# Performance work log

Measured on AMD Instinct MI355X. Metric: run time of the kernel, lower is better.

The kernel has to match this reference:

```python
import jax, jax.numpy as jnp
import numpy as np

B, L, C, H, W = 2, 3, 64, 32, 32
DI, N, DT_RANK, K = 128, 16, 4, 4  # d_inner=2*C, d_state, dt_rank=ceil(C/16), 4 scan dirs


def setup_inputs() -> dict:
    key = jax.random.key(0)
    ks = iter(jax.random.split(key, 48))
    nrm = lambda shape, s=0.02: jax.random.normal(next(ks), shape, jnp.float32) * s
    return {
        "image_sequence": jax.random.normal(next(ks), (B, L, C, H, W), jnp.float32),
        "difficult_zone": jax.random.normal(next(ks), (B, C, H, W), jnp.float32),
        "sigma": jax.random.uniform(next(ks), (B, C, H, W), jnp.float32),
        # LayerNorm2d applied to each frame
        "norm_g": jnp.ones((C,)), "norm_b": jnp.zeros((C,)),
        # ConvolutionalResBlock (in=3C -> out=C), GroupNorm(num_groups=1)
        "gn1_g": jnp.ones((3 * C,)), "gn1_b": jnp.zeros((3 * C,)),
        "conv1_w": nrm((C, 3 * C, 3, 3)), "conv1_b": jnp.zeros((C,)),
        "gn2_g": jnp.ones((C,)), "gn2_b": jnp.zeros((C,)),
        "conv2_w": nrm((C, C, 3, 3)), "conv2_b": jnp.zeros((C,)),
        "skip_w": nrm((C, 3 * C, 1, 1)), "skip_b": jnp.zeros((C,)),
        # VSSBlock pre-norms
        "ln1_g": jnp.ones((C,)), "ln1_b": jnp.zeros((C,)),
        "ln2_g": jnp.ones((C,)), "ln2_b": jnp.zeros((C,)),
        # SS2D
        "in_proj_w": nrm((2 * DI, C)),
        "dwconv_w": nrm((DI, 1, 3, 3)), "dwconv_b": jnp.zeros((DI,)),
        "x_proj_w": nrm((K, DT_RANK + 2 * N, DI)),
        "dt_proj_w": nrm((K, DI, DT_RANK), 0.1),
        "dt_proj_b": jnp.log(jnp.expm1(jnp.full((K, DI), 0.01, jnp.float32))),
        "A_logs": jnp.log(jnp.tile(jnp.arange(1, N + 1, dtype=jnp.float32), (K * DI, 1))),
        "Ds": jnp.ones((K * DI,)),
        "out_norm_g": jnp.ones((DI,)), "out_norm_b": jnp.zeros((DI,)),
        "out_proj_w": nrm((C, DI)),
        # Mlp (hidden = C)
        "fc1_w": nrm((C, C)), "fc1_b": jnp.zeros((C,)),
        "fc2_w": nrm((C, C)), "fc2_b": jnp.zeros((C,)),
    }


def _ln(x, g, b, eps=1e-5):  # layernorm over last axis
    m = x.mean(-1, keepdims=True)
    v = x.var(-1, keepdims=True)
    return (x - m) * jax.lax.rsqrt(v + eps) * g + b


def _ln2d(x, g, b, eps=1e-6):  # per-pixel channel layernorm, NCHW
    m = x.mean(1, keepdims=True)
    v = x.var(1, keepdims=True)
    return (x - m) * jax.lax.rsqrt(v + eps) * g[None, :, None, None] + b[None, :, None, None]


def _gn1(x, g, b, eps=1e-5):  # GroupNorm(num_groups=1), NCHW
    m = x.mean((1, 2, 3), keepdims=True)
    v = x.var((1, 2, 3), keepdims=True)
    return (x - m) * jax.lax.rsqrt(v + eps) * g[None, :, None, None] + b[None, :, None, None]


def _conv(x, w, b, pad):
    y = jax.lax.conv_general_dilated(x, w, (1, 1), [(pad, pad), (pad, pad)],
                                     dimension_numbers=("NCHW", "OIHW", "NCHW"))
    return y + b[None, :, None, None]


def _forward(image_sequence, difficult_zone, sigma, norm_g, norm_b, gn1_g, gn1_b,
             conv1_w, conv1_b, gn2_g, gn2_b, conv2_w, conv2_b, skip_w, skip_b,
             ln1_g, ln1_b, ln2_g, ln2_b, in_proj_w, dwconv_w, dwconv_b, x_proj_w,
             dt_proj_w, dt_proj_b, A_logs, Ds, out_norm_g, out_norm_b, out_proj_w,
             fc1_w, fc1_b, fc2_w, fc2_b):
    b, l, c, h, w = image_sequence.shape
    bl, L2 = b * l, h * w
    # fold frame loop into batch (identical math per frame in the torch loop)
    frames = _ln2d(image_sequence.reshape(bl, c, h, w), norm_g, norm_b)
    dz = jnp.broadcast_to(difficult_zone[:, None], (b, l, c, h, w)).reshape(bl, c, h, w)
    sg = jnp.broadcast_to(sigma[:, None], (b, l, c, h, w)).reshape(bl, c, h, w)
    x = jnp.concatenate([dz, frames, sg], axis=1)  # [bl, 3c, h, w]
    # channel compressor: pre-act conv res block
    hdn = _conv(jax.nn.silu(_gn1(x, gn1_g, gn1_b)), conv1_w, conv1_b, 1)
    hdn = _conv(jax.nn.silu(_gn1(hdn, gn2_g, gn2_b)), conv2_w, conv2_b, 1)
    x = hdn + _conv(x, skip_w, skip_b, 0)          # [bl, c, h, w]
    x = x.transpose(0, 2, 3, 1)                    # [bl, h, w, c]
    # --- VSSBlock (pre-norm): x = x + SS2D(LN(x)) ---
    xn = _ln(x, ln1_g, ln1_b)
    xz = xn @ in_proj_w.T                          # [bl,h,w,2*DI]
    xc, z = jnp.split(xz, 2, axis=-1)
    xc = xc.transpose(0, 3, 1, 2)                  # [bl, DI, h, w]
    xc = jax.lax.conv_general_dilated(xc, dwconv_w, (1, 1), [(1, 1), (1, 1)],
                                      dimension_numbers=("NCHW", "OIHW", "NCHW"),
                                      feature_group_count=DI) + dwconv_b[None, :, None, None]
    xc = jax.nn.silu(xc)
    # 4-direction scan inputs (HW, WH, and their reverses)
    xf = xc.reshape(bl, DI, L2)
    xt = xc.transpose(0, 1, 3, 2).reshape(bl, DI, L2)
    xs = jnp.stack([xf, xt], axis=1)
    xs = jnp.concatenate([xs, jnp.flip(xs, axis=-1)], axis=1)  # [bl, 4, DI, L2]
    x_dbl = jnp.einsum("bkdl,kcd->bkcl", xs, x_proj_w)
    dts, Bs, Cs = jnp.split(x_dbl, [DT_RANK, DT_RANK + N], axis=2)
    dts = jnp.einsum("bkrl,kdr->bkdl", dts, dt_proj_w) + dt_proj_b[None, :, :, None]
    dts = jax.nn.softplus(dts)                     # [bl, 4, DI, L2]
    A = -jnp.exp(A_logs).reshape(K, DI, N)
    dA = jnp.exp(dts[..., None] * A[None, :, :, None, :])            # [bl,4,DI,L2,N]
    dBu = dts[..., None] * Bs.transpose(0, 1, 3, 2)[:, :, None] * xs[..., None]
    a_t = dA.transpose(3, 0, 1, 2, 4)              # [L2, bl, 4, DI, N]
    bu_t = dBu.transpose(3, 0, 1, 2, 4)
    c_t = Cs.transpose(3, 0, 1, 2)                 # [L2, bl, 4, N]

    def step(hid, inp):
        a_i, bu_i, c_i = inp
        hid = a_i * hid + bu_i
        return hid, jnp.einsum("bkdn,bkn->bkd", hid, c_i)

    h0 = jnp.zeros((bl, K, DI, N), xs.dtype)
    _, ys = jax.lax.scan(step, h0, (a_t, bu_t, c_t))                 # [L2, bl, 4, DI]
    ys = ys.transpose(1, 2, 3, 0) + xs * Ds.reshape(K, DI)[None, :, :, None]
    inv = jnp.flip(ys[:, 2:4], axis=-1)
    y = (ys[:, 0] + inv[:, 0]
         + ys[:, 1].reshape(bl, DI, w, h).transpose(0, 1, 3, 2).reshape(bl, DI, L2)
         + inv[:, 1].reshape(bl, DI, w, h).transpose(0, 1, 3, 2).reshape(bl, DI, L2))
    y = _ln(y.transpose(0, 2, 1), out_norm_g, out_norm_b).reshape(bl, h, w, DI)
    y = y * jax.nn.silu(z)
    x = x + y @ out_proj_w.T
    # --- x = x + Mlp(LN(x)) ---
    xn = _ln(x, ln2_g, ln2_b)
    x = x + (jax.nn.gelu(xn @ fc1_w.T + fc1_b, approximate=False) @ fc2_w.T + fc2_b)
    return x.transpose(0, 3, 1, 2).reshape(b, l, c, h, w)


def reference(image_sequence, difficult_zone, sigma, norm_g, norm_b, gn1_g, gn1_b,
              conv1_w, conv1_b, gn2_g, gn2_b, conv2_w, conv2_b, skip_w, skip_b,
              ln1_g, ln1_b, ln2_g, ln2_b, in_proj_w, dwconv_w, dwconv_b, x_proj_w,
              dt_proj_w, dt_proj_b, A_logs, Ds, out_norm_g, out_norm_b, out_proj_w,
              fc1_w, fc1_b, fc2_w, fc2_b):
    return _forward(image_sequence, difficult_zone, sigma, norm_g, norm_b, gn1_g, gn1_b,
                    conv1_w, conv1_b, gn2_g, gn2_b, conv2_w, conv2_b, skip_w, skip_b,
                    ln1_g, ln1_b, ln2_g, ln2_b, in_proj_w, dwconv_w, dwconv_b, x_proj_w,
                    dt_proj_w, dt_proj_b, A_logs, Ds, out_norm_g, out_norm_b, out_proj_w,
                    fc1_w, fc1_b, fc2_w, fc2_b)
```

## Files before the change

kernel.cpp:

```cpp
#include <hip/hip_runtime.h>
#include <math.h>

#define BL    6
#define CCH   64
#define C3    192
#define L2    1024
#define DIC   128
#define NST   16
#define K4    4
#define PSTR  1088
#define NCH   32

#define LOG2E 1.44269504088896340736f
#define LN2C  0.69314718055994530942f

typedef float f2 __attribute__((ext_vector_type(2)));
__device__ __forceinline__ f2 mkf2(float a, float b){ f2 r; r.x=a; r.y=b; return r; }
__device__ __forceinline__ f2 fma2(f2 a, float b, f2 c){
  f2 bb; bb.x=b; bb.y=b;
  return __builtin_elementwise_fma(a, bb, c);
}

__device__ __forceinline__ float fexp(float x){ return __builtin_amdgcn_exp2f(x*LOG2E); }
__device__ __forceinline__ float fsilu(float x){ return x * __builtin_amdgcn_rcpf(1.f + fexp(-x)); }
__device__ __forceinline__ float fsoftplus(float x){
  if (x > 20.f) return x;
  return __builtin_amdgcn_logf(1.f + fexp(x)) * LN2C;
}
__device__ __forceinline__ float fgelu(float x){
  return 0.5f*x*(1.f + erff(x*0.70710678118654752440f));
}

__global__ __launch_bounds__(256) void k_ln2d(const float* __restrict__ img,
    const float* __restrict__ dz, const float* __restrict__ sg,
    const float* __restrict__ g, const float* __restrict__ b, float* __restrict__ x3c,
    float* __restrict__ psum1, float* __restrict__ psq1){
  __shared__ float ps[4][8], pq[4][8], gs[4], gq[4];
  int s = blockIdx.x >> 7;
  int pg = blockIdx.x & 127;
  int tid = threadIdx.x;
  int px = tid & 7; int cg = tid >> 3;
  int wv = tid >> 6; int lane = tid & 63;
  int p = pg*8 + px;
  int bsmp = s/3;
  const float* fr = img + (size_t)s*CCH*L2;
  float vals[2]; float sm=0.f, sq=0.f;
  #pragma unroll
  for (int j=0;j<2;++j){
    int c = cg*2 + j;
    float v = fr[c*L2 + p];
    vals[j]=v; sm+=v; sq+=v*v;
  }
  sm += __shfl_xor(sm,8,64);  sq += __shfl_xor(sq,8,64);
  sm += __shfl_xor(sm,16,64); sq += __shfl_xor(sq,16,64);
  sm += __shfl_xor(sm,32,64); sq += __shfl_xor(sq,32,64);
  if (lane < 8){ ps[wv][lane]=sm; pq[wv][lane]=sq; }
  __syncthreads();
  sm = ps[0][px]+ps[1][px]+ps[2][px]+ps[3][px];
  sq = pq[0][px]+pq[1][px]+pq[2][px]+pq[3][px];
  float mean = sm*(1.f/CCH); float var = sq*(1.f/CCH)-mean*mean;
  float rs = rsqrtf(var + 1e-6f);
  float* o = x3c + (size_t)s*C3*L2;
  const float* dzp = dz + (size_t)bsmp*CCH*L2;
  const float* sgp = sg + (size_t)bsmp*CCH*L2;
  float gsm=0.f, gsq=0.f;
  #pragma unroll
  for (int j=0;j<2;++j){
    int c = cg*2+j;
    float dzv = dzp[c*L2+p];
    float nv  = (vals[j]-mean)*rs*g[c] + b[c];
    float sgv = sgp[c*L2+p];
    o[c*L2+p] = dzv;
    o[(CCH+c)*L2+p] = nv;
    o[(2*CCH+c)*L2+p] = sgv;
    gsm += dzv+nv+sgv; gsq += dzv*dzv+nv*nv+sgv*sgv;
  }
  for (int m=1;m<64;m<<=1){ gsm+=__shfl_xor(gsm,m,64); gsq+=__shfl_xor(gsq,m,64); }
  if (lane==0){ gs[wv]=gsm; gq[wv]=gsq; }
  __syncthreads();
  if (tid==0){
    psum1[blockIdx.x] = gs[0]+gs[1]+gs[2]+gs[3];
    psq1 [blockIdx.x] = gq[0]+gq[1]+gq[2]+gq[3];
  }
}

__global__ __launch_bounds__(256) void k_gnact1_skip(const float* __restrict__ x3c,
    const float* __restrict__ psum, const float* __restrict__ psq,
    const float* __restrict__ g, const float* __restrict__ b,
    const float* __restrict__ wsk,
    float* __restrict__ xact1, float* __restrict__ part){
  int bx = blockIdx.x;
  int tid = threadIdx.x;
  if (bx < 1152){
    int s = bx / C3; int c = bx % C3;
    float sm=0.f, sq=0.f;
    for (int i=0;i<128;++i){ sm += psum[s*128+i]; sq += psq[s*128+i]; }
    float mean = sm*(1.f/(C3*L2));
    float var = sq*(1.f/(C3*L2)) - mean*mean;
    float rs = rsqrtf(var + 1e-5f);
    float gc = g[c]*rs; float bc = b[c] - mean*rs*g[c];
    float4 v = *(const float4*)(x3c + (size_t)bx*1024 + tid*4);
    float4 o; o.x = fsilu(v.x*gc+bc); o.y = fsilu(v.y*gc+bc);
    o.z = fsilu(v.z*gc+bc); o.w = fsilu(v.w*gc+bc);
    float* pl = xact1 + (size_t)bx*PSTR;
    *(float4*)(pl + 32 + tid*4) = o;
    float4 z4 = make_float4(0.f,0.f,0.f,0.f);
    if (tid < 8)  *(float4*)(pl + tid*4) = z4;
    else if (tid < 16) *(float4*)(pl + 1056 + (tid-8)*4) = z4;
  } else {
    int t = bx - 1152;
    int role = t & 1; int cop = (t>>1)&31; int s = t >> 6;
    int co0 = cop*2, co1 = co0+1;
    int row = tid>>3; int q = tid&7; int col0 = q*4;
    int p = row*32+col0;
    f2 a[4];
    #pragma unroll
    for (int i=0;i<4;++i){ a[i].x=0.f; a[i].y=0.f; }
    int ci0 = role*96;
    const float* x3 = x3c + ((size_t)s*C3 + ci0)*L2 + p;
    const float* w0p = wsk + co0*C3 + ci0;
    const float* w1p = wsk + co1*C3 + ci0;
    #pragma unroll 4
    for (int ci=0; ci<96; ++ci){
      float4 v = *(const float4*)(x3 + (size_t)ci*L2);
      f2 w = mkf2(w0p[ci], w1p[ci]);
      a[0] = fma2(w, v.x, a[0]);
      a[1] = fma2(w, v.y, a[1]);
      a[2] = fma2(w, v.z, a[2]);
      a[3] = fma2(w, v.w, a[3]);
    }
    float* pp = part + (size_t)(4+role)*(BL*CCH*L2) + ((size_t)s*CCH+co0)*L2 + p;
    *(float4*)pp = make_float4(a[0].x,a[1].x,a[2].x,a[3].x);
    *(float4*)(pp+L2) = make_float4(a[0].y,a[1].y,a[2].y,a[3].y);
  }
}

__global__ __launch_bounds__(256) void k_gnact_pad(const float* __restrict__ x,
    const float* __restrict__ psum, const float* __restrict__ psq,
    const float* __restrict__ g, const float* __restrict__ b,
    int ch, int parts, float inv_n, float eps, float* __restrict__ out){
  int bx = blockIdx.x;
  int s = bx / ch; int c = bx % ch;
  int tid = threadIdx.x;
  float sm=0.f, sq=0.f;
  for (int i=0;i<parts;++i){ sm += psum[s*parts+i]; sq += psq[s*parts+i]; }
  float mean = sm*inv_n;
  float var = sq*inv_n - mean*mean;
  float rs = rsqrtf(var + eps);
  float gc = g[c]*rs; float bc = b[c] - mean*rs*g[c];
  float4 v = *(const float4*)(x + (size_t)bx*1024 + tid*4);
  float4 o; o.x = fsilu(v.x*gc+bc); o.y = fsilu(v.y*gc+bc);
  o.z = fsilu(v.z*gc+bc); o.w = fsilu(v.w*gc+bc);
  float* pl = out + (size_t)bx*PSTR;
  *(float4*)(pl + 32 + tid*4) = o;
  float4 z4 = make_float4(0.f,0.f,0.f,0.f);
  if (tid < 8)  *(float4*)(pl + tid*4) = z4;
  else if (tid < 16) *(float4*)(pl + 1056 + (tid-8)*4) = z4;
}

__device__ __forceinline__ void conv_row_acc2(f2* a, float4 mid, float lf, float rt,
    const float* wp0, const float* wp1){
  f2 w0 = mkf2(wp0[0],wp1[0]);
  f2 w1 = mkf2(wp0[1],wp1[1]);
  f2 w2 = mkf2(wp0[2],wp1[2]);
  a[0] = fma2(w0,lf,   fma2(w1,mid.x, fma2(w2,mid.y, a[0])));
  a[1] = fma2(w0,mid.x,fma2(w1,mid.y, fma2(w2,mid.z, a[1])));
  a[2] = fma2(w0,mid.y,fma2(w1,mid.z, fma2(w2,mid.w, a[2])));
  a[3] = fma2(w0,mid.z,fma2(w1,mid.w, fma2(w2,rt,    a[3])));
}

__device__ __forceinline__ void conv_ci_body2(float4 m0, float4 m1, float4 m2, int q,
    const float* wp0, const float* wp1, f2* a){
  float lf0=__shfl_up(m0.w,1,64), rt0=__shfl_down(m0.x,1,64);
  float lf1=__shfl_up(m1.w,1,64), rt1=__shfl_down(m1.x,1,64);
  float lf2=__shfl_up(m2.w,1,64), rt2=__shfl_down(m2.x,1,64);
  if (q==0){ lf0=0.f; lf1=0.f; lf2=0.f; }
  if (q==7){ rt0=0.f; rt1=0.f; rt2=0.f; }
  conv_row_acc2(a,m0,lf0,rt0, wp0+0, wp1+0);
  conv_row_acc2(a,m1,lf1,rt1, wp0+3, wp1+3);
  conv_row_acc2(a,m2,lf2,rt2, wp0+6, wp1+6);
}

__global__ __launch_bounds__(256) void k_conv1_split(const float* __restrict__ xact,
    const float* __restrict__ w, float* __restrict__ part){
  int bx = blockIdx.x; int kk = bx % 12; int r = bx / 12;
  int cop = r & 31; int s = r >> 5;
  int co0 = cop*2, co1 = co0+1;
  int tid = threadIdx.x; int row = tid>>3; int q = tid&7; int col0 = q*4;
  f2 a[4];
  #pragma unroll
  for (int i=0;i<4;++i){ a[i].x=0.f; a[i].y=0.f; }
  int ci0 = kk*16;
  const float* pl = xact + ((size_t)s*C3 + ci0)*PSTR + row*32 + col0;
  const float* wp0 = w + (size_t)(co0*C3 + ci0)*9;
  const float* wp1 = w + (size_t)(co1*C3 + ci0)*9;
  float4 m0 = *(const float4*)(pl);
  float4 m1 = *(const float4*)(pl+32);
  float4 m2 = *(const float4*)(pl+64);
  #pragma unroll 2
  for (int i=0;i<16;++i){
    const float* pn = pl + (i<15 ? PSTR : 0);
    float4 n0 = *(const float4*)(pn);
    float4 n1 = *(const float4*)(pn+32);
    float4 n2 = *(const float4*)(pn+64);
    conv_ci_body2(m0,m1,m2,q, wp0, wp1, a);
    wp0 += 9; wp1 += 9; pl = pn; m0=n0; m1=n1; m2=n2;
  }
  float* pp = part + (size_t)kk*(BL*CCH*L2) + ((size_t)s*CCH+co0)*L2 + row*32+col0;
  *(float4*)pp = make_float4(a[0].x,a[1].x,a[2].x,a[3].x);
  *(float4*)(pp+L2) = make_float4(a[0].y,a[1].y,a[2].y,a[3].y);
}

__global__ __launch_bounds__(256) void k_reduce1(const float* __restrict__ part,
    const float* __restrict__ bias, float* __restrict__ h1,
    float* __restrict__ psum2, float* __restrict__ psq2){
  int co = blockIdx.x & 63; int s = blockIdx.x >> 6;
  size_t ofs = ((size_t)s*CCH+co)*L2 + threadIdx.x*4;
  const size_t stride = (size_t)BL*CCH*L2;
  float4 acc = *(const float4*)(part + ofs);
  #pragma unroll
  for (int kk=1;kk<12;++kk){
    float4 r = *(const float4*)(part + (size_t)kk*stride + ofs);
    acc.x += r.x; acc.y += r.y; acc.z += r.z; acc.w += r.w;
  }
  float bv = bias[co];
  acc.x += bv; acc.y += bv; acc.z += bv; acc.w += bv;
  *(float4*)(h1 + ofs) = acc;
  float sm = acc.x+acc.y+acc.z+acc.w;
  float sq = acc.x*acc.x+acc.y*acc.y+acc.z*acc.z+acc.w*acc.w;
  for (int m=1;m<64;m<<=1){ sm+=__shfl_xor(sm,m,64); sq+=__shfl_xor(sq,m,64); }
  __shared__ float s_sm[4], s_sq[4];
  int wv = threadIdx.x>>6;
  if ((threadIdx.x&63)==0){ s_sm[wv]=sm; s_sq[wv]=sq; }
  __syncthreads();
  if (threadIdx.x==0){
    psum2[blockIdx.x] = s_sm[0]+s_sm[1]+s_sm[2]+s_sm[3];
    psq2 [blockIdx.x] = s_sq[0]+s_sq[1]+s_sq[2]+s_sq[3];
  }
}

__global__ __launch_bounds__(256) void k_conv2_split(const float* __restrict__ xact2,
    const float* __restrict__ w2, float* __restrict__ part){
  int bx = blockIdx.x; int role = bx & 3; int t = bx >> 2;
  int cop = t & 31; int s = t >> 5;
  int co0 = cop*2, co1 = co0+1;
  int tid = threadIdx.x; int row = tid>>3; int q = tid&7; int col0 = q*4;
  int p = row*32+col0;
  f2 a[4];
  #pragma unroll
  for (int i=0;i<4;++i){ a[i].x=0.f; a[i].y=0.f; }
  int ci0 = role*16;
  const float* pl = xact2 + ((size_t)s*CCH + ci0)*PSTR + row*32 + col0;
  const float* wp0 = w2 + (size_t)(co0*CCH + ci0)*9;
  const float* wp1 = w2 + (size_t)(co1*CCH + ci0)*9;
  float4 m0 = *(const float4*)(pl);
  float4 m1 = *(const float4*)(pl+32);
  float4 m2 = *(const float4*)(pl+64);
  #pragma unroll 2
  for (int i=0;i<16;++i){
    const float* pn = pl + (i<15 ? PSTR : 0);
    float4 n0 = *(const float4*)(pn);
    float4 n1 = *(const float4*)(pn+32);
    float4 n2 = *(const float4*)(pn+64);
    conv_ci_body2(m0,m1,m2,q, wp0, wp1, a);
    wp0 += 9; wp1 += 9; pl = pn; m0=n0; m1=n1; m2=n2;
  }
  float* pp = part + (size_t)role*(BL*CCH*L2) + ((size_t)s*CCH+co0)*L2 + p;
  *(float4*)pp = make_float4(a[0].x,a[1].x,a[2].x,a[3].x);
  *(float4*)(pp+L2) = make_float4(a[0].y,a[1].y,a[2].y,a[3].y);
}

__global__ __launch_bounds__(256) void k_red2_ln1_inproj(const float* __restrict__ part,
    const float* __restrict__ b2, const float* __restrict__ bsk,
    const float* __restrict__ g, const float* __restrict__ b,
    const float* __restrict__ W,
    float* __restrict__ x_cmaj, float* __restrict__ xc, float* __restrict__ z_t){
  __shared__ float xn_s[64*65];
  int bx = blockIdx.x; int oq = bx & 7; int pg = (bx>>3)&15; int s = bx>>7;
  int p0 = pg*64;
  int tid = threadIdx.x;
  const size_t stride = (size_t)BL*CCH*L2;
  #pragma unroll
  for (int kq=0;kq<4;++kq){
    int f = kq*256 + tid;
    int co = f >> 4; int px4 = (f & 15)*4;
    size_t ofs = ((size_t)s*CCH+co)*L2 + p0 + px4;
    float4 r0 = *(const float4*)(part + ofs);
    float4 r1 = *(const float4*)(part + stride + ofs);
    float4 r2 = *(const float4*)(part + 2*stride + ofs);
    float4 r3 = *(const float4*)(part + 3*stride + ofs);
    float4 r4 = *(const float4*)(part + 4*stride + ofs);
    float4 r5 = *(const float4*)(part + 5*stride + ofs);
    float bv = b2[co]+bsk[co];
    float4 o;
    o.x = ((r0.x+r1.x)+(r2.x+r3.x))+(r4.x+r5.x)+bv;
    o.y = ((r0.y+r1.y)+(r2.y+r3.y))+(r4.y+r5.y)+bv;
    o.z = ((r0.z+r1.z)+(r2.z+r3.z))+(r4.z+r5.z)+bv;
    o.w = ((r0.w+r1.w)+(r2.w+r3.w))+(r4.w+r5.w)+bv;
    if (oq == 0) *(float4*)(x_cmaj + ofs) = o;
    xn_s[(px4+0)*65 + co] = o.x;
    xn_s[(px4+1)*65 + co] = o.y;
    xn_s[(px4+2)*65 + co] = o.z;
    xn_s[(px4+3)*65 + co] = o.w;
  }
  __syncthreads();
  {
    int wv = __builtin_amdgcn_readfirstlane(tid>>6); int lane = tid&63;
    for (int j=0;j<16;++j){
      int pl = wv*16 + j;
      float v = xn_s[pl*65 + lane];
      float sm = v, sq = v*v;
      for (int m=1;m<64;m<<=1){ sm += __shfl_xor(sm,m,64); sq += __shfl_xor(sq,m,64); }
      float mean = sm*(1.f/64.f); float var = sq*(1.f/64.f) - mean*mean;
      float rs = rsqrtf(var + 1e-5f);
      xn_s[pl*65 + lane] = (v-mean)*rs*g[lane] + b[lane];
    }
  }
  __syncthreads();
  int px_l = tid & 63;
  int og = __builtin_amdgcn_readfirstlane(tid >> 6);
  int o0 = oq*32 + og*8;
  f2 acc[4];
  #pragma unroll
  for (int oi=0;oi<4;++oi){ acc[oi].x=0.f; acc[oi].y=0.f; }
  for (int c=0;c<64;++c){
    float xv = xn_s[px_l*65 + c];
    #pragma unroll
    for (int oi=0;oi<4;++oi)
      acc[oi] = fma2(mkf2(W[(o0+2*oi)*64 + c], W[(o0+2*oi+1)*64 + c]), xv, acc[oi]);
  }
  int p = p0 + px_l;
  if (oq < 4){
    #pragma unroll
    for (int oi=0;oi<4;++oi){
      xc[((size_t)s*DIC + o0 + 2*oi)*L2 + p]   = acc[oi].x;
      xc[((size_t)s*DIC + o0 + 2*oi+1)*L2 + p] = acc[oi].y;
    }
  } else {
    #pragma unroll
    for (int oi=0;oi<4;++oi){
      z_t[((size_t)s*DIC + (o0-128) + 2*oi)*L2 + p]   = acc[oi].x;
      z_t[((size_t)s*DIC + (o0-128) + 2*oi+1)*L2 + p] = acc[oi].y;
    }
  }
}

__global__ __launch_bounds__(256) void k_xproj_dt(const float* __restrict__ xc,
    const float* __restrict__ dww, const float* __restrict__ dwb,
    const float* __restrict__ W,
    float* __restrict__ dtr, float* __restrict__ Bp, float* __restrict__ Cp,
    float* __restrict__ u_t){
  __shared__ float smem[128*68];
  int bx = blockIdx.x; int pg = bx & 15; int sk = bx >> 4;
  int k = sk & 3; int s = sk >> 2;
  int tid = threadIdx.x;
  for (int i = tid; i < 128*16; i += 256){
    int dr = i>>4; int j4 = (i&15)*4;
    int rw = j4>>5; int col0 = j4 & 31;
    int gr = pg*2 + rw;
    int q = i&7;
    const float* xr = xc + ((size_t)s*DIC+dr)*L2;
    const float* wp = dww + dr*9;
    float bv = dwb[dr];
    float4 acc = make_float4(bv,bv,bv,bv);
    #pragma unroll
    for (int dy=-1;dy<=1;++dy){
      int r = gr+dy;
      float4 mid = make_float4(0.f,0.f,0.f,0.f);
      if (0<=r && r<32) mid = *(const float4*)(xr + r*32 + col0);
      float lf = __shfl_up(mid.w,1,64); if(q==0) lf=0.f;
      float rt = __shfl_down(mid.x,1,64); if(q==7) rt=0.f;
      float w0=wp[(dy+1)*3], w1=wp[(dy+1)*3+1], w2=wp[(dy+1)*3+2];
      acc.x = fmaf(w0,lf,   fmaf(w1,mid.x, fmaf(w2,mid.y, acc.x)));
      acc.y = fmaf(w0,mid.x,fmaf(w1,mid.y, fmaf(w2,mid.z, acc.y)));
      acc.z = fmaf(w0,mid.y,fmaf(w1,mid.z, fmaf(w2,mid.w, acc.z)));
      acc.w = fmaf(w0,mid.z,fmaf(w1,mid.w, fmaf(w2,rt,    acc.w)));
    }
    acc.x = fsilu(acc.x); acc.y = fsilu(acc.y); acc.z = fsilu(acc.z); acc.w = fsilu(acc.w);
    *(float4*)&smem[dr*68 + j4] = acc;
  }
  __syncthreads();
  if (k == 0){
    float* ub = u_t + ((size_t)(s*L2) + pg*64)*DIC;
    for (int i = tid; i < 64*128; i += 256){
      int px2 = i>>7; int dd = i&127;
      ub[(size_t)px2*DIC + dd] = smem[dd*68 + px2];
    }
  }
  int px = tid & 63;
  int cgrp = __builtin_amdgcn_readfirstlane(tid >> 6);
  int c0 = cgrp*9;
  const float* wb = W + (size_t)(k*36 + c0)*DIC;
  f2 acc2[4]; float acc8 = 0.f;
  #pragma unroll
  for (int ci=0;ci<4;++ci){ acc2[ci].x=0.f; acc2[ci].y=0.f; }
  for (int d=0; d<DIC; ++d){
    float xv = smem[d*68 + px];
    #pragma unroll
    for (int ci=0;ci<4;++ci)
      acc2[ci] = fma2(mkf2(wb[(2*ci)*DIC+d], wb[(2*ci+1)*DIC+d]), xv, acc2[ci]);
    acc8 = fmaf(wb[8*DIC+d], xv, acc8);
  }
  __syncthreads();
  #pragma unroll
  for (int ci=0;ci<4;++ci){
    smem[(c0+2*ci)*68 + px]   = acc2[ci].x;
    smem[(c0+2*ci+1)*68 + px] = acc2[ci].y;
  }
  smem[(c0+8)*68 + px] = acc8;
  __syncthreads();
  {
    int pp = tid >> 2; int r = tid & 3;
    dtr[((size_t)sk*L2 + pg*64 + pp)*4 + r] = smem[r*68 + pp];
  }
  float* Bb = Bp + ((size_t)sk*L2 + pg*64)*NST;
  float* Cb = Cp + ((size_t)sk*L2 + pg*64)*NST;
  for (int i = tid; i < 1024; i += 256){
    int pp = i>>4; int n = i&15;
    Bb[pp*NST + n] = smem[(4+n)*68 + pp];
    Cb[pp*NST + n] = smem[(20+n)*68 + pp];
  }
}

__device__ __forceinline__ int scan_pix32(int ch, int j, int k){
  if (k==0) return ch*32 + j;
  if (k==1) return j*32 + ch;
  if (k==2) return 1023 - (ch*32 + j);
  return 1023 - (j*32 + ch);
}

struct StepH { float4 dt4; float uv; float4 B0,B1; };
__device__ __forceinline__ StepH loadH(const float* dr, const float* ub, const float* Bb, int p){
  StepH r;
  r.dt4 = *(const float4*)(dr + (size_t)p*4);
  r.uv = ub[(size_t)p*DIC];
  const float* bp = Bb + p*NST;
  r.B0 = *(const float4*)bp; r.B1 = *(const float4*)(bp+4);
  return r;
}
__device__ __forceinline__ float dt_eval(float4 w4, float bb, float4 d4){
  return fsoftplus(fmaf(w4.x,d4.x,fmaf(w4.y,d4.y,fmaf(w4.z,d4.z,fmaf(w4.w,d4.w,bb)))));
}

__device__ __forceinline__ bool aco_linear(const float* aco, float acoR, int gbase){
  bool ok = true;
  #pragma unroll
  for (int n=0;n<8;++n){
    float ideal = (float)(gbase+n+1) * acoR;
    ok = ok && (fabsf(aco[n]-ideal) <= 1e-5f*fabsf(ideal) + 1e-12f);
  }
  return ok;
}

__global__ __launch_bounds__(256,4) void k_scan_part3(const float* __restrict__ dtr,
    const float* __restrict__ dtw, const float* __restrict__ dtb,
    const float* __restrict__ u_t, const float* __restrict__ Bp,
    const float* __restrict__ A_logs, float* __restrict__ hend, float* __restrict__ Ssum){
  int bx = blockIdx.x; int ch = bx & 31; int sk = bx >> 5;
  int k = sk & 3; int s = sk >> 2;
  int tid = threadIdx.x; int d = tid >> 1; int nh = tid & 1;
  float aco[8];
  float acoR = -LOG2E * fexp(A_logs[(size_t)(k*DIC+d)*NST]);
  {
    const float* ab = A_logs + (size_t)(k*DIC+d)*NST + nh*8;
    #pragma unroll
    for (int n=0;n<8;++n) aco[n] = -LOG2E * fexp(ab[n]);
  }
  bool fast = aco_linear(aco, acoR, nh*8);
  float aco0 = aco[0];
  float4 w4 = *(const float4*)(dtw + (size_t)(k*DIC+d)*4);
  float bb = dtb[k*DIC+d];
  float h[8]; float Sacc = 0.f;
  #pragma unroll
  for (int n=0;n<8;++n) h[n]=0.f;
  const float* dr = dtr + (size_t)sk*L2*4;
  const float* ub = u_t + (size_t)s*L2*DIC + d;
  const float* Bb = Bp + (size_t)sk*L2*NST + nh*8;
  StepH cur = loadH(dr, ub, Bb, scan_pix32(ch, 0, k));
  if (fast){
    #pragma unroll 4
    for (int j=0;j<32;++j){
      StepH nxt;
      if (j < 31) nxt = loadH(dr, ub, Bb, scan_pix32(ch, j+1, k));
      float dtv = dt_eval(w4, bb, cur.dt4);
      Sacc += dtv;
      float tv = dtv*cur.uv;
      float rr = __builtin_amdgcn_exp2f(dtv*acoR);
      float a_ = __builtin_amdgcn_exp2f(dtv*aco0);
      h[0] = fmaf(a_, h[0], tv*cur.B0.x);
      a_ *= rr; h[1] = fmaf(a_, h[1], tv*cur.B0.y);
      a_ *= rr; h[2] = fmaf(a_, h[2], tv*cur.B0.z);
      a_ *= rr; h[3] = fmaf(a_, h[3], tv*cur.B0.w);
      a_ *= rr; h[4] = fmaf(a_, h[4], tv*cur.B1.x);
      a_ *= rr; h[5] = fmaf(a_, h[5], tv*cur.B1.y);
      a_ *= rr; h[6] = fmaf(a_, h[6], tv*cur.B1.z);
      a_ *= rr; h[7] = fmaf(a_, h[7], tv*cur.B1.w);
      cur = nxt;
    }
  } else {
    #pragma unroll 4
    for (int j=0;j<32;++j){
      StepH nxt;
      if (j < 31) nxt = loadH(dr, ub, Bb, scan_pix32(ch, j+1, k));
      float dtv = dt_eval(w4, bb, cur.dt4);
      Sacc += dtv;
      float tv = dtv*cur.uv;
      #define PSTEP(NI, BV) { float a_ = __builtin_amdgcn_exp2f(dtv*aco[NI]); \
        h[NI] = fmaf(a_, h[NI], tv*(BV)); }
      PSTEP(0,cur.B0.x) PSTEP(1,cur.B0.y) PSTEP(2,cur.B0.z) PSTEP(3,cur.B0.w)
      PSTEP(4,cur.B1.x) PSTEP(5,cur.B1.y) PSTEP(6,cur.B1.z) PSTEP(7,cur.B1.w)
      #undef PSTEP
      cur = nxt;
    }
  }
  size_t base = ((size_t)(sk*NCH + ch)*DIC + d)*NST + nh*8;
  *(float4*)(hend + base)     = make_float4(h[0],h[1],h[2],h[3]);
  *(float4*)(hend + base + 4) = make_float4(h[4],h[5],h[6],h[7]);
  if (nh == 0) Ssum[(size_t)(sk*NCH + ch)*DIC + d] = Sacc;
}

__global__ __launch_bounds__(256) void k_scan_fix3(const float* __restrict__ hend,
    const float* __restrict__ Ssum, const float* __restrict__ A_logs,
    float* __restrict__ Hin){
  int t = blockIdx.x*256 + threadIdx.x;
  int n = t & 15; int d = (t>>4) & 127; int sk = t >> 11; int k = sk & 3;
  float aco = -LOG2E * fexp(A_logs[(size_t)(k*DIC+d)*NST + n]);
  float H = 0.f;
  #pragma unroll 8
  for (int ch=0; ch<NCH; ++ch){
    size_t sidx = (size_t)(sk*NCH + ch)*DIC + d;
    float pa = __builtin_amdgcn_exp2f(aco * Ssum[sidx]);
    float he = hend[sidx*NST + n];
    Hin[sidx*NST + n] = H;
    H = fmaf(pa, H, he);
  }
}

__global__ __launch_bounds__(256,4) void k_scan_y3(const float* __restrict__ dtr,
    const float* __restrict__ dtw, const float* __restrict__ dtb,
    const float* __restrict__ u_t, const float* __restrict__ Bp, const float* __restrict__ Cp,
    const float* __restrict__ A_logs, const float* __restrict__ Ds,
    const float* __restrict__ Hin, float* __restrict__ ys_t){
  int bx = blockIdx.x; int ch = bx & 31; int sk = bx >> 5;
  int k = sk & 3; int s = sk >> 2;
  int tid = threadIdx.x; int d = tid >> 1; int nh = tid & 1;
  float aco[8];
  float acoR = -LOG2E * fexp(A_logs[(size_t)(k*DIC+d)*NST]);
  {
    const float* ab = A_logs + (size_t)(k*DIC+d)*NST + nh*8;
    #pragma unroll
    for (int n=0;n<8;++n) aco[n] = -LOG2E * fexp(ab[n]);
  }
  bool fast = aco_linear(aco, acoR, nh*8);
  float aco0 = aco[0];
  float4 w4 = *(const float4*)(dtw + (size_t)(k*DIC+d)*4);
  float bb = dtb[k*DIC+d];
  float Dv = Ds[k*DIC+d];
  float h[8];
  size_t hbase = ((size_t)(sk*NCH + ch)*DIC + d)*NST + nh*8;
  {
    float4 h0 = *(const float4*)(Hin + hbase);
    float4 h1 = *(const float4*)(Hin + hbase + 4);
    h[0]=h0.x; h[1]=h0.y; h[2]=h0.z; h[3]=h0.w;
    h[4]=h1.x; h[5]=h1.y; h[6]=h1.z; h[7]=h1.w;
  }
  const float* dr = dtr + (size_t)sk*L2*4;
  const float* ub = u_t + (size_t)s*L2*DIC + d;
  const float* Bb = Bp + (size_t)sk*L2*NST + nh*8;
  const float* Cb = Cp + (size_t)sk*L2*NST + nh*8;
  float* yb = ys_t + (size_t)sk*L2*DIC + d;
  int pcur = scan_pix32(ch, 0, k);
  StepH cur = loadH(dr, ub, Bb, pcur);
  float4 Cc0 = *(const float4*)(Cb + pcur*NST);
  float4 Cc1 = *(const float4*)(Cb + pcur*NST + 4);
  if (fast){
    #pragma unroll 4
    for (int j=0;j<32;++j){
      StepH nxt; float4 Cn0, Cn1; int pn = pcur;
      if (j < 31){
        pn = scan_pix32(ch, j+1, k);
        nxt = loadH(dr, ub, Bb, pn);
        Cn0 = *(const float4*)(Cb + pn*NST);
        Cn1 = *(const float4*)(Cb + pn*NST + 4);
      }
      float dtv = dt_eval(w4, bb, cur.dt4);
      float tv = dtv*cur.uv;
      float y0=0.f, y1=0.f, y2=0.f, y3=0.f;
      float rr = __builtin_amdgcn_exp2f(dtv*acoR);
      float a_ = __builtin_amdgcn_exp2f(dtv*aco0);
      h[0] = fmaf(a_, h[0], tv*cur.B0.x); y0 = fmaf(h[0], Cc0.x, y0);
      a_ *= rr; h[1] = fmaf(a_, h[1], tv*cur.B0.y); y1 = fmaf(h[1], Cc0.y, y1);
      a_ *= rr; h[2] = fmaf(a_, h[2], tv*cur.B0.z); y2 = fmaf(h[2], Cc0.z, y2);
      a_ *= rr; h[3] = fmaf(a_, h[3], tv*cur.B0.w); y3 = fmaf(h[3], Cc0.w, y3);
      a_ *= rr; h[4] = fmaf(a_, h[4], tv*cur.B1.x); y0 = fmaf(h[4], Cc1.x, y0);
      a_ *= rr; h[5] = fmaf(a_, h[5], tv*cur.B1.y); y1 = fmaf(h[5], Cc1.y, y1);
      a_ *= rr; h[6] = fmaf(a_, h[6], tv*cur.B1.z); y2 = fmaf(h[6], Cc1.z, y2);
      a_ *= rr; h[7] = fmaf(a_, h[7], tv*cur.B1.w); y3 = fmaf(h[7], Cc1.w, y3);
      float py = (y0+y1)+(y2+y3);
      float tot = py + __shfl_xor(py, 1, 64);
      if (nh == 0) yb[(size_t)pcur*DIC] = fmaf(cur.uv, Dv, tot);
      cur = nxt; Cc0 = Cn0; Cc1 = Cn1; pcur = pn;
    }
  } else {
    #pragma unroll 4
    for (int j=0;j<32;++j){
      StepH nxt; float4 Cn0, Cn1; int pn = pcur;
      if (j < 31){
        pn = scan_pix32(ch, j+1, k);
        nxt = loadH(dr, ub, Bb, pn);
        Cn0 = *(const float4*)(Cb + pn*NST);
        Cn1 = *(const float4*)(Cb + pn*NST + 4);
      }
      float dtv = dt_eval(w4, bb, cur.dt4);
      float tv = dtv*cur.uv;
      float y0=0.f, y1=0.f, y2=0.f, y3=0.f;
      #define YSTEP(NI, BV, CV, YA) { float a_ = __builtin_amdgcn_exp2f(dtv*aco[NI]); \
        h[NI] = fmaf(a_, h[NI], tv*(BV)); YA = fmaf(h[NI], (CV), YA); }
      YSTEP(0,cur.B0.x,Cc0.x,y0) YSTEP(1,cur.B0.y,Cc0.y,y1) YSTEP(2,cur.B0.z,Cc0.z,y2) YSTEP(3,cur.B0.w,Cc0.w,y3)
      YSTEP(4,cur.B1.x,Cc1.x,y0) YSTEP(5,cur.B1.y,Cc1.y,y1) YSTEP(6,cur.B1.z,Cc1.z,y2) YSTEP(7,cur.B1.w,Cc1.w,y3)
      #undef YSTEP
      float py = (y0+y1)+(y2+y3);
      float tot = py + __shfl_xor(py, 1, 64);
      if (nh == 0) yb[(size_t)pcur*DIC] = fmaf(cur.uv, Dv, tot);
      cur = nxt; Cc0 = Cn0; Cc1 = Cn1; pcur = pn;
    }
  }
}

__global__ __launch_bounds__(256) void k_tail(const float* __restrict__ ys_t,
    const float* __restrict__ z_t, const float* __restrict__ ong, const float* __restrict__ onb,
    const float* __restrict__ Wop, const float* __restrict__ x_cmaj,
    const float* __restrict__ g2, const float* __restrict__ b2n,
    const float* __restrict__ w1, const float* __restrict__ b1,
    const float* __restrict__ w2, const float* __restrict__ b2,
    float* __restrict__ out){
  __shared__ float yt[128*9];
  __shared__ float xvt[64*9];
  __shared__ float ts[64*9];
  int s = blockIdx.x >> 7; int pg = blockIdx.x & 127;
  int tid = threadIdx.x;
  {
    int wv = __builtin_amdgcn_readfirstlane(tid>>6); int lane = tid&63;
    int d0 = lane, d1 = lane+64;
    for (int i=0;i<2;++i){
      int px = i*4 + wv; int p = pg*8 + px;
      const float* yb = ys_t + ((size_t)(s*4)*L2 + p)*DIC;
      float ya = yb[d0] + yb[(size_t)L2*DIC + d0] + yb[(size_t)2*L2*DIC + d0] + yb[(size_t)3*L2*DIC + d0];
      float yc = yb[d1] + yb[(size_t)L2*DIC + d1] + yb[(size_t)2*L2*DIC + d1] + yb[(size_t)3*L2*DIC + d1];
      float sm = ya+yc, sq = ya*ya+yc*yc;
      for (int m=1;m<64;m<<=1){ sm+=__shfl_xor(sm,m,64); sq+=__shfl_xor(sq,m,64); }
      float mean = sm*(1.f/128.f); float var = sq*(1.f/128.f)-mean*mean;
      float rs = rsqrtf(var + 1e-5f);
      float yn0 = (ya-mean)*rs*ong[d0] + onb[d0];
      float yn1 = (yc-mean)*rs*ong[d1] + onb[d1];
      float zv0 = z_t[((size_t)s*DIC+d0)*L2 + p];
      float zv1 = z_t[((size_t)s*DIC+d1)*L2 + p];
      yt[d0*9 + px] = yn0 * fsilu(zv0);
      yt[d1*9 + px] = yn1 * fsilu(zv1);
    }
  }
  __syncthreads();
  {
    int px = tid & 7; int cgp = tid >> 3;
    int c0 = cgp*2;
    f2 A; A.x=0.f; A.y=0.f;
    for (int d=0; d<DIC; ++d){
      float yv = yt[d*9 + px];
      A = fma2(mkf2(Wop[(c0+0)*DIC + d], Wop[(c0+1)*DIC + d]), yv, A);
    }
    int p = pg*8 + px;
    size_t base = ((size_t)s*CCH + c0)*L2 + p;
    xvt[(c0+0)*9 + px] = x_cmaj[base]    + A.x;
    xvt[(c0+1)*9 + px] = x_cmaj[base+L2] + A.y;
  }
  __syncthreads();
  int px = tid & 7; int cgp = tid >> 3;
  float sm=0.f, sq=0.f;
  for (int c=0;c<64;++c){ float v = xvt[c*9+px]; sm+=v; sq+=v*v; }
  float mean = sm*(1.f/64.f);
  float rs = rsqrtf(sq*(1.f/64.f) - mean*mean + 1e-5f);
  int o0 = cgp*2;
  f2 T = mkf2(b1[o0], b1[o0+1]);
  for (int c=0;c<64;++c){
    float xn = (xvt[c*9+px]-mean)*rs*g2[c] + b2n[c];
    T = fma2(mkf2(w1[(o0+0)*64 + c], w1[(o0+1)*64 + c]), xn, T);
  }
  ts[(o0+0)*9 + px] = fgelu(T.x);
  ts[(o0+1)*9 + px] = fgelu(T.y);
  __syncthreads();
  int c0 = cgp*2;
  f2 ACC = mkf2(xvt[(c0+0)*9+px] + b2[c0+0], xvt[(c0+1)*9+px] + b2[c0+1]);
  for (int o=0;o<64;++o){
    float tv = ts[o*9+px];
    ACC = fma2(mkf2(w2[(c0+0)*64 + o], w2[(c0+1)*64 + o]), tv, ACC);
  }
  int p = pg*8 + px;
  out[((size_t)s*CCH + c0+0)*L2 + p] = ACC.x;
  out[((size_t)s*CCH + c0+1)*L2 + p] = ACC.y;
}

extern "C" void kernel_launch(void* const* d_in, const int* in_sizes, int n_in,
                              void* d_out, int out_size, void* d_ws, size_t ws_size,
                              hipStream_t stream){
  (void)in_sizes; (void)n_in; (void)out_size; (void)ws_size;
  const float* img      = (const float*)d_in[0];
  const float* dz       = (const float*)d_in[1];
  const float* sg       = (const float*)d_in[2];
  const float* norm_g   = (const float*)d_in[3];
  const float* norm_b   = (const float*)d_in[4];
  const float* gn1_g    = (const float*)d_in[5];
  const float* gn1_b    = (const float*)d_in[6];
  const float* conv1_w  = (const float*)d_in[7];
  const float* conv1_b  = (const float*)d_in[8];
  const float* gn2_g    = (const float*)d_in[9];
  const float* gn2_b    = (const float*)d_in[10];
  const float* conv2_w  = (const float*)d_in[11];
  const float* conv2_b  = (const float*)d_in[12];
  const float* skip_w   = (const float*)d_in[13];
  const float* skip_b   = (const float*)d_in[14];
  const float* ln1_g    = (const float*)d_in[15];
  const float* ln1_b    = (const float*)d_in[16];
  const float* ln2_g    = (const float*)d_in[17];
  const float* ln2_b    = (const float*)d_in[18];
  const float* in_proj_w= (const float*)d_in[19];
  const float* dwconv_w = (const float*)d_in[20];
  const float* dwconv_b = (const float*)d_in[21];
  const float* x_proj_w = (const float*)d_in[22];
  const float* dt_proj_w= (const float*)d_in[23];
  const float* dt_proj_b= (const float*)d_in[24];
  const float* A_logs   = (const float*)d_in[25];
  const float* Ds       = (const float*)d_in[26];
  const float* out_norm_g = (const float*)d_in[27];
  const float* out_norm_b = (const float*)d_in[28];
  const float* out_proj_w = (const float*)d_in[29];
  const float* fc1_w    = (const float*)d_in[30];
  const float* fc1_b    = (const float*)d_in[31];
  const float* fc2_w    = (const float*)d_in[32];
  const float* fc2_b    = (const float*)d_in[33];

  float* ws = (float*)d_ws;
  float* x3c    = ws;
  float* xact1  = x3c    + 1179648;
  float* h1     = xact1  + 1253376;
  float* xact2  = h1     + 393216;
  float* xpslot = xact2  + 417792;
  float* x_cmaj = xpslot + 393216;
  float* z_t    = x_cmaj + 393216;
  float* xc     = z_t    + 786432;
  float* cpslot = xc     + 786432;
  float* hole   = cpslot + 786432;
  float* scanbuf= hole   + 884736;
  float* ys_t   = scanbuf+ 3145728;
  float* statsb = ys_t   + 3145728;
  float* psum1  = statsb;
  float* psq1   = statsb + 768;
  float* psum2  = statsb + 1536;
  float* psq2   = statsb + 1920;
  float* part1  = scanbuf;
  float* part2  = ys_t;
  float* hend   = x3c;
  float* u_t    = h1;
  float* Bp     = xpslot;
  float* Cp     = cpslot;
  float* dtr    = hole;
  float* Ssum   = hole + 98304;
  float* Hin    = scanbuf;

  k_ln2d<<<768, 256, 0, stream>>>(img, dz, sg, norm_g, norm_b, x3c, psum1, psq1);
  k_gnact1_skip<<<1536, 256, 0, stream>>>(x3c, psum1, psq1, gn1_g, gn1_b, skip_w,
                                          xact1, part2);
  k_conv1_split<<<2304, 256, 0, stream>>>(xact1, conv1_w, part1);
  k_reduce1<<<384, 256, 0, stream>>>(part1, conv1_b, h1, psum2, psq2);
  k_gnact_pad<<<6*CCH, 256, 0, stream>>>(h1, psum2, psq2, gn2_g, gn2_b, CCH, 64,
                                         1.f/(CCH*L2), 1e-5f, xact2);
  k_conv2_split<<<768, 256, 0, stream>>>(xact2, conv2_w, part2);
  k_red2_ln1_inproj<<<768, 256, 0, stream>>>(part2, conv2_b, skip_b, ln1_g, ln1_b, in_proj_w,
                                             x_cmaj, xc, z_t);
  k_xproj_dt<<<384, 256, 0, stream>>>(xc, dwconv_w, dwconv_b, x_proj_w, dtr, Bp, Cp, u_t);
  k_scan_part3<<<768, 256, 0, stream>>>(dtr, dt_proj_w, dt_proj_b, u_t, Bp, A_logs, hend, Ssum);
  k_scan_fix3<<<192, 256, 0, stream>>>(hend, Ssum, A_logs, Hin);
  k_scan_y3<<<768, 256, 0, stream>>>(dtr, dt_proj_w, dt_proj_b, u_t, Bp, Cp, A_logs, Ds, Hin, ys_t);
  k_tail<<<768, 256, 0, stream>>>(ys_t, z_t, out_norm_g, out_norm_b, out_proj_w, x_cmaj,
                                  ln2_g, ln2_b, fc1_w, fc1_b, fc2_w, fc2_b, (float*)d_out);
}
```

Before: 286.4 us.

## Split xproj across two blocks and fold chunk-prefix fixup into scan_y

The x_proj kernel now launches twice as many blocks. One half computes the dt/B rows, the other computes the C rows and writes u_t, which raises parallelism at the cost of recomputing the depthwise conv in both halves. The separate k_scan_fix3 kernel is removed. Each k_scan_y3 block now rebuilds its incoming chunk state by serially combining the hend/Ssum of all earlier chunks, which saves a launch and the Hin round-trip but adds redundant work that grows with the chunk index.

```diff
diff --git a/kernel.cpp b/kernel.cpp
--- a/kernel.cpp
+++ b/kernel.cpp
@@ -351,7 +351,7 @@
     float* __restrict__ dtr, float* __restrict__ Bp, float* __restrict__ Cp,
     float* __restrict__ u_t){
   __shared__ float smem[128*68];
-  int bx = blockIdx.x; int pg = bx & 15; int sk = bx >> 4;
+  int bx = blockIdx.x; int half = bx & 1; int pg = (bx>>1) & 15; int sk = bx >> 5;
   int k = sk & 3; int s = sk >> 2;
   int tid = threadIdx.x;
   for (int i = tid; i < 128*16; i += 256){
@@ -380,45 +380,63 @@
     *(float4*)&smem[dr*68 + j4] = acc;
   }
   __syncthreads();
-  if (k == 0){
-    float* ub = u_t + ((size_t)(s*L2) + pg*64)*DIC;
-    for (int i = tid; i < 64*128; i += 256){
-      int px2 = i>>7; int dd = i&127;
-      ub[(size_t)px2*DIC + dd] = smem[dd*68 + px2];
-    }
-  }
   int px = tid & 63;
   int cgrp = __builtin_amdgcn_readfirstlane(tid >> 6);
-  int c0 = cgrp*9;
-  const float* wb = W + (size_t)(k*36 + c0)*DIC;
-  f2 acc2[4]; float acc8 = 0.f;
-  #pragma unroll
-  for (int ci=0;ci<4;++ci){ acc2[ci].x=0.f; acc2[ci].y=0.f; }
-  for (int d=0; d<DIC; ++d){
-    float xv = smem[d*68 + px];
-    #pragma unroll
-    for (int ci=0;ci<4;++ci)
-      acc2[ci] = fma2(mkf2(wb[(2*ci)*DIC+d], wb[(2*ci+1)*DIC+d]), xv, acc2[ci]);
-    acc8 = fmaf(wb[8*DIC+d], xv, acc8);
-  }
-  __syncthreads();
-  #pragma unroll
-  for (int ci=0;ci<4;++ci){
-    smem[(c0+2*ci)*68 + px]   = acc2[ci].x;
-    smem[(c0+2*ci+1)*68 + px] = acc2[ci].y;
-  }
-  smem[(c0+8)*68 + px] = acc8;
-  __syncthreads();
-  {
-    int pp = tid >> 2; int r = tid & 3;
-    dtr[((size_t)sk*L2 + pg*64 + pp)*4 + r] = smem[r*68 + pp];
-  }
-  float* Bb = Bp + ((size_t)sk*L2 + pg*64)*NST;
-  float* Cb = Cp + ((size_t)sk*L2 + pg*64)*NST;
-  for (int i = tid; i < 1024; i += 256){
-    int pp = i>>4; int n = i&15;
-    Bb[pp*NST + n] = smem[(4+n)*68 + pp];
-    Cb[pp*NST + n] = smem[(20+n)*68 + pp];
+  if (half == 1){
+    if (k == 0){
+      float* ub = u_t + ((size_t)(s*L2) + pg*64)*DIC;
+      for (int i = tid; i < 64*128; i += 256){
+        int px2 = i>>7; int dd = i&127;
+        ub[(size_t)px2*DIC + dd] = smem[dd*68 + px2];
+      }
+    }
+    int c0 = 20 + cgrp*4;
+    const float* wb = W + (size_t)(k*36 + c0)*DIC;
+    f2 acc2[2];
+    acc2[0].x=0.f; acc2[0].y=0.f; acc2[1].x=0.f; acc2[1].y=0.f;
+    for (int d=0; d<DIC; ++d){
+      float xv = smem[d*68 + px];
+      acc2[0] = fma2(mkf2(wb[0*DIC+d], wb[1*DIC+d]), xv, acc2[0]);
+      acc2[1] = fma2(mkf2(wb[2*DIC+d], wb[3*DIC+d]), xv, acc2[1]);
+    }
+    __syncthreads();
+    smem[(c0+0)*68 + px] = acc2[0].x;
+    smem[(c0+1)*68 + px] = acc2[0].y;
+    smem[(c0+2)*68 + px] = acc2[1].x;
+    smem[(c0+3)*68 + px] = acc2[1].y;
+    __syncthreads();
+    float* Cb = Cp + ((size_t)sk*L2 + pg*64)*NST;
+    for (int i = tid; i < 1024; i += 256){
+      int pp = i>>4; int n = i&15;
+      Cb[pp*NST + n] = smem[(20+n)*68 + pp];
+    }
+  } else {
+    int c0 = cgrp*5;
+    const float* wb = W + (size_t)(k*36 + c0)*DIC;
+    f2 acc2[2]; float acc4 = 0.f;
+    acc2[0].x=0.f; acc2[0].y=0.f; acc2[1].x=0.f; acc2[1].y=0.f;
+    for (int d=0; d<DIC; ++d){
+      float xv = smem[d*68 + px];
+      acc2[0] = fma2(mkf2(wb[0*DIC+d], wb[1*DIC+d]), xv, acc2[0]);
+      acc2[1] = fma2(mkf2(wb[2*DIC+d], wb[3*DIC+d]), xv, acc2[1]);
+      acc4 = fmaf(wb[4*DIC+d], xv, acc4);
+    }
+    __syncthreads();
+    smem[(c0+0)*68 + px] = acc2[0].x;
+    smem[(c0+1)*68 + px] = acc2[0].y;
+    smem[(c0+2)*68 + px] = acc2[1].x;
+    smem[(c0+3)*68 + px] = acc2[1].y;
+    smem[(c0+4)*68 + px] = acc4;
+    __syncthreads();
+    {
+      int pp = tid >> 2; int r = tid & 3;
+      dtr[((size_t)sk*L2 + pg*64 + pp)*4 + r] = smem[r*68 + pp];
+    }
+    float* Bb = Bp + ((size_t)sk*L2 + pg*64)*NST;
+    for (int i = tid; i < 1024; i += 256){
+      int pp = i>>4; int n = i&15;
+      Bb[pp*NST + n] = smem[(4+n)*68 + pp];
+    }
   }
 }
 
@@ -519,28 +537,12 @@
   if (nh == 0) Ssum[(size_t)(sk*NCH + ch)*DIC + d] = Sacc;
 }
 
-__global__ __launch_bounds__(256) void k_scan_fix3(const float* __restrict__ hend,
-    const float* __restrict__ Ssum, const float* __restrict__ A_logs,
-    float* __restrict__ Hin){
-  int t = blockIdx.x*256 + threadIdx.x;
-  int n = t & 15; int d = (t>>4) & 127; int sk = t >> 11; int k = sk & 3;
-  float aco = -LOG2E * fexp(A_logs[(size_t)(k*DIC+d)*NST + n]);
-  float H = 0.f;
-  #pragma unroll 8
-  for (int ch=0; ch<NCH; ++ch){
-    size_t sidx = (size_t)(sk*NCH + ch)*DIC + d;
-    float pa = __builtin_amdgcn_exp2f(aco * Ssum[sidx]);
-    float he = hend[sidx*NST + n];
-    Hin[sidx*NST + n] = H;
-    H = fmaf(pa, H, he);
-  }
-}
-
 __global__ __launch_bounds__(256,4) void k_scan_y3(const float* __restrict__ dtr,
     const float* __restrict__ dtw, const float* __restrict__ dtb,
     const float* __restrict__ u_t, const float* __restrict__ Bp, const float* __restrict__ Cp,
     const float* __restrict__ A_logs, const float* __restrict__ Ds,
-    const float* __restrict__ Hin, float* __restrict__ ys_t){
+    const float* __restrict__ hend, const float* __restrict__ Ssum,
+    float* __restrict__ ys_t){
   int bx = blockIdx.x; int ch = bx & 31; int sk = bx >> 5;
   int k = sk & 3; int s = sk >> 2;
   int tid = threadIdx.x; int d = tid >> 1; int nh = tid & 1;
@@ -557,12 +559,35 @@
   float bb = dtb[k*DIC+d];
   float Dv = Ds[k*DIC+d];
   float h[8];
-  size_t hbase = ((size_t)(sk*NCH + ch)*DIC + d)*NST + nh*8;
+  #pragma unroll
+  for (int n=0;n<8;++n) h[n]=0.f;
   {
-    float4 h0 = *(const float4*)(Hin + hbase);
-    float4 h1 = *(const float4*)(Hin + hbase + 4);
-    h[0]=h0.x; h[1]=h0.y; h[2]=h0.z; h[3]=h0.w;
-    h[4]=h1.x; h[5]=h1.y; h[6]=h1.z; h[7]=h1.w;
+    const float* Sb = Ssum + (size_t)sk*NCH*DIC + d;
+    const float* Hb = hend + ((size_t)sk*NCH*DIC + d)*NST + nh*8;
+    for (int cc=0; cc<ch; ++cc){
+      float Sv = Sb[(size_t)cc*DIC];
+      float4 e0 = *(const float4*)(Hb + (size_t)cc*DIC*NST);
+      float4 e1 = *(const float4*)(Hb + (size_t)cc*DIC*NST + 4);
+      if (fast){
+        float rr = __builtin_amdgcn_exp2f(acoR*Sv);
+        float a_ = __builtin_amdgcn_exp2f(aco0*Sv);
+        h[0] = fmaf(a_, h[0], e0.x);
+        a_ *= rr; h[1] = fmaf(a_, h[1], e0.y);
+        a_ *= rr; h[2] = fmaf(a_, h[2], e0.z);
+        a_ *= rr; h[3] = fmaf(a_, h[3], e0.w);
+        a_ *= rr; h[4] = fmaf(a_, h[4], e1.x);
+        a_ *= rr; h[5] = fmaf(a_, h[5], e1.y);
+        a_ *= rr; h[6] = fmaf(a_, h[6], e1.z);
+        a_ *= rr; h[7] = fmaf(a_, h[7], e1.w);
+      } else {
+        float he[8] = {e0.x,e0.y,e0.z,e0.w,e1.x,e1.y,e1.z,e1.w};
+        #pragma unroll
+        for (int n=0;n<8;++n){
+          float pa = __builtin_amdgcn_exp2f(aco[n]*Sv);
+          h[n] = fmaf(pa, h[n], he[n]);
+        }
+      }
+    }
   }
   const float* dr = dtr + (size_t)sk*L2*4;
   const float* ub = u_t + (size_t)s*L2*DIC + d;
@@ -764,7 +789,6 @@
   float* Cp     = cpslot;
   float* dtr    = hole;
   float* Ssum   = hole + 98304;
-  float* Hin    = scanbuf;
 
   k_ln2d<<<768, 256, 0, stream>>>(img, dz, sg, norm_g, norm_b, x3c, psum1, psq1);
   k_gnact1_skip<<<1536, 256, 0, stream>>>(x3c, psum1, psq1, gn1_g, gn1_b, skip_w,
@@ -776,10 +800,10 @@
   k_conv2_split<<<768, 256, 0, stream>>>(xact2, conv2_w, part2);
   k_red2_ln1_inproj<<<768, 256, 0, stream>>>(part2, conv2_b, skip_b, ln1_g, ln1_b, in_proj_w,
                                              x_cmaj, xc, z_t);
-  k_xproj_dt<<<384, 256, 0, stream>>>(xc, dwconv_w, dwconv_b, x_proj_w, dtr, Bp, Cp, u_t);
+  k_xproj_dt<<<768, 256, 0, stream>>>(xc, dwconv_w, dwconv_b, x_proj_w, dtr, Bp, Cp, u_t);
   k_scan_part3<<<768, 256, 0, stream>>>(dtr, dt_proj_w, dt_proj_b, u_t, Bp, A_logs, hend, Ssum);
-  k_scan_fix3<<<192, 256, 0, stream>>>(hend, Ssum, A_logs, Hin);
-  k_scan_y3<<<768, 256, 0, stream>>>(dtr, dt_proj_w, dt_proj_b, u_t, Bp, Cp, A_logs, Ds, Hin, ys_t);
+  k_scan_y3<<<768, 256, 0, stream>>>(dtr, dt_proj_w, dt_proj_b, u_t, Bp, Cp, A_logs, Ds,
+                                     hend, Ssum, ys_t);
   k_tail<<<768, 256, 0, stream>>>(ys_t, z_t, out_norm_g, out_norm_b, out_proj_w, x_cmaj,
                                   ln2_g, ln2_b, fc1_w, fc1_b, fc2_w, fc2_b, (float*)d_out);
 }
```

Measured after the change: 288.2 us, median of 2. No clear change (+0.6%).
